# Performance work log

Measured on AMD Instinct MI355X. Metric: run time of the kernel, lower is better.

## Reference

```python
import jax, jax.numpy as jnp
import numpy as np

WS = 128          # crop window size
EPS = 1e-06


def setup_inputs() -> dict:
    key = jax.random.key(0)
    ks = jax.random.split(key, 8)
    E, S, K, H, W, HID = 32, 2, 256, 384, 384, 128
    x = jax.random.normal(ks[0], (E, H, W), jnp.float32)
    sigma = jax.random.uniform(ks[1], (S, H, W), jnp.float32)
    c = jax.random.normal(ks[2], (K, E), jnp.float32)
    centroids = jax.random.randint(ks[3], (K, 2), 0, H).astype(jnp.int32)
    M = jax.random.uniform(ks[4], (K, K), jnp.float32)  # sigmoid affinities in [0,1]
    din = E + S
    W1 = jax.random.normal(ks[5], (din, HID), jnp.float32) / np.sqrt(din)
    W2 = jax.random.normal(ks[6], (HID, HID), jnp.float32) / np.sqrt(HID)
    W3 = jax.random.normal(ks[7], (HID, 1), jnp.float32) / np.sqrt(HID)
    return {"x": x, "sigma": sigma, "c": c, "centroids": centroids, "M": M,
            "W1": W1, "b1": jnp.zeros((HID,), jnp.float32),
            "W2": W2, "b2": jnp.zeros((HID,), jnp.float32),
            "W3": W3, "b3": jnp.zeros((1,), jnp.float32)}


def reference(x, sigma, c, M, W1, b1, W2, b2, W3, b3, centroids):
    E, h, w = x.shape
    K = c.shape[0]
    ws, half = WS, WS // 2

    # ---- centre_crop: per-seed clamped top-left + mesh-grid indices ----
    cy = jnp.clip(centroids[:, 0], half, h - half)           # [K]
    cx = jnp.clip(centroids[:, 1], half, w - half)
    ty, tx = cy - half, cx - half                             # top-left (y, x)
    ar = jnp.arange(ws, dtype=jnp.int32)
    gy = jnp.broadcast_to(ty[:, None, None] + ar[None, :, None], (K, ws, ws))
    gx = jnp.broadcast_to(tx[:, None, None] + ar[None, None, :], (K, ws, ws))

    # ---- feature_engineering: gather crops, subtract seed embedding ----
    feats = jnp.concatenate([x, sigma], axis=0)               # [E+S, h, w]
    crops = feats[:, gy, gx]                                  # [E+S, K, ws, ws]
    crops = jnp.moveaxis(crops, 0, 1)                         # [K, E+S, ws, ws]
    crops = crops.at[:, :E].add(-c[:, :, None, None])

    # ---- pixel_classifier: per-pixel MLP -> logit ----
    pix = jnp.moveaxis(crops, 1, -1)                          # [K, ws, ws, E+S]
    h1 = jax.nn.relu(pix @ W1 + b1)
    h2 = jax.nn.relu(h1 @ W2 + b2)
    dist = (h2 @ W3 + b3)[..., 0]                             # [K, ws, ws]

    # ---- _gate_by_center_logit: logit(sig(a)*sig(b)) = a+b-softplus(logaddexp(a,b)) ----
    cyi = (centroids[:, 0] - ty).astype(jnp.int32)
    cxi = (centroids[:, 1] - tx).astype(jnp.int32)
    center = dist[jnp.arange(K), cyi, cxi]                    # [K]
    b = center[:, None, None]
    dist = dist + b - jax.nn.softplus(jnp.logaddexp(dist, b))

    # ---- apply_seed_merging: scatter to [K, h*w], affinity-weighted merge, gather ----
    Ms = 0.5 * (M + M.T)
    Ms = Ms.at[jnp.diag_indices(K)].set(1.0)
    pix_idx = (gy * w + gx).reshape(K, ws * ws)               # unique within each crop
    rows = jnp.arange(K)[:, None]
    logits = jnp.zeros((K, h * w), dist.dtype).at[rows, pix_idx].set(dist.reshape(K, -1))
    has = jnp.zeros((K, h * w), dist.dtype).at[rows, pix_idx].set(1.0)
    merged = (Ms @ logits) / jnp.clip(Ms @ has, EPS, None)
    out = merged[rows, pix_idx].reshape(K, 1, ws, ws)
    return out
```

## Files before the change

### kernel.cpp

```cpp
#include <hip/hip_runtime.h>
#include <hip/hip_bf16.h>


#define HH    384
#define WW    384
#define NE    32
#define NK    256
#define HALF  64
#define HWSZ  (HH * WW)
#define EPSV  1e-6f
#define CAPX  192

typedef _Float16 half8 __attribute__((ext_vector_type(8)));
typedef _Float16 half2v __attribute__((ext_vector_type(2)));
typedef float floatx4 __attribute__((ext_vector_type(4)));

#define MFMA16(a, b, c) __builtin_amdgcn_mfma_f32_16x16x32_f16((a), (b), (c), 0, 0, 0)

__device__ __forceinline__ half2v pk_f16(float a, float b) {
    return __builtin_bit_cast(half2v, __builtin_amdgcn_cvt_pkrtz(a, b));
}

__device__ __forceinline__ int row_order(int ri) {
    return (ri & 1) ? (191 - (ri >> 1)) : (192 + (ri >> 1));
}

#define WS_DIST   0
#define WS_MSYM   4194304
#define WS_W2F    4259840
#define WS_D      4268032
#define WS_CENTER 4284416
#define WS_G      5026560

__global__ void prep_kernel(const float* __restrict__ M, const float* __restrict__ W1,
                            const float* __restrict__ W2, const float* __restrict__ c,
                            const float* __restrict__ b1,
                            float* __restrict__ Msym, _Float16* __restrict__ W2f,
                            _Float16* __restrict__ D) {
    int idx = blockIdx.x * 256 + threadIdx.x;
    {
        int i = idx >> 8, j = idx & 255;
        Msym[idx] = (i == j) ? 1.0f : 0.5f * (M[i * NK + j] + M[j * NK + i]);
    }
    if (idx < 2048) {
        int l = idx & 63;
        int col = ((idx >> 8) << 4) + (l & 15);
        int kb = ((idx >> 6) & 3) * 32 + 8 * (l >> 4);
        #pragma unroll
        for (int j = 0; j < 8; ++j)
            W2f[idx * 8 + j] = (_Float16)W2[(kb + j) * 128 + col];
    }
    if (idx < 32768) {
        int k = idx >> 7, h = idx & 127;
        float s = -b1[h];
        #pragma unroll 8
        for (int e = 0; e < NE; ++e) s = fmaf(c[k * NE + e], W1[e * 128 + h], s);
        D[idx] = (_Float16)s;
    }
}

__global__ __launch_bounds__(256)
void gfeat_kernel(const float* __restrict__ x, const float* __restrict__ sigma,
                  const float* __restrict__ W1, _Float16* __restrict__ G) {
    int px = blockIdx.x * 256 + threadIdx.x;
    float f[34];
    #pragma unroll
    for (int e = 0; e < NE; ++e) f[e] = x[e * HWSZ + px];
    f[32] = sigma[px];
    f[33] = sigma[HWSZ + px];
    _Float16* gp = G + (size_t)px * 128;
    #pragma unroll 1
    for (int h0 = 0; h0 < 128; h0 += 8) {
        half8 hv;
        #pragma unroll
        for (int j = 0; j < 8; ++j) {
            float z = 0.0f;
            const float* w1 = W1 + (h0 + j);
            #pragma unroll
            for (int e = 0; e < 34; ++e) z = fmaf(f[e], w1[e * 128], z);
            hv[j] = (_Float16)z;
        }
        *(half8*)(gp + h0) = hv;
    }
}

__global__ __launch_bounds__(128)
void center2_kernel(const _Float16* __restrict__ G, const _Float16* __restrict__ D,
                    const float* __restrict__ W2, const float* __restrict__ b2,
                    const float* __restrict__ W3, const float* __restrict__ b3,
                    const int* __restrict__ cent, float* __restrict__ center) {
    __shared__ float h1s[128];
    __shared__ float red[2];
    int k = blockIdx.x, j = threadIdx.x;
    int cy0 = cent[2 * k], cx0 = cent[2 * k + 1];
    const _Float16* g = G + ((size_t)cy0 * WW + cx0) * 128;
    h1s[j] = fmaxf((float)g[j] - (float)D[k * 128 + j], 0.0f);
    __syncthreads();
    float acc = 0.0f;
    #pragma unroll 8
    for (int i = 0; i < 128; ++i) acc = fmaf(h1s[i], W2[i * 128 + j], acc);
    float p = fmaxf(acc + b2[j], 0.0f) * W3[j];
    #pragma unroll
    for (int m = 1; m < 64; m <<= 1) p += __shfl_xor(p, m, 64);
    if ((j & 63) == 0) red[j >> 6] = p;
    __syncthreads();
    if (j == 0) center[k] = red[0] + red[1] + b3[0];
}

__global__ __launch_bounds__(256)
void pix_kernel(const _Float16* __restrict__ G, const _Float16* __restrict__ D,
                const _Float16* __restrict__ W2f, const int* __restrict__ cent,
                const float* __restrict__ b2, const float* __restrict__ W3,
                const float* __restrict__ b3, const float* __restrict__ center,
                float* __restrict__ dist) {
    __shared__ int   sjw[CAPX];
    __shared__ float sctr[CAPX];
    __shared__ int   scnt;

    const int tid = threadIdx.x;
    const int l   = tid & 63;
    const int wv  = tid >> 6;
    const int lg  = l >> 4;
    const int xi  = l & 15;

    const int r   = row_order(blockIdx.x / 6);
    const int xt  = blockIdx.x % 6;
    const int wx0 = xt * 64 + wv * 16;

    if (wv == 0) {
        int base = 0;
        const int2* c2 = (const int2*)cent;
        #pragma unroll
        for (int cch = 0; cch < 4; ++cch) {
            int j = cch * 64 + l;
            int2 cc = c2[j];
            int ty = min(max(cc.x, HALF), HH - HALF) - HALF;
            int tx = min(max(cc.y, HALF), WW - HALF) - HALF;
            bool f = (r >= ty) && (r < ty + 128) &&
                     (tx <= xt * 64 + 63) && (tx + 127 >= xt * 64);
            unsigned long long m = __ballot(f);
            int pos = base + __popcll(m & ((1ull << l) - 1ull));
            if (f && pos < CAPX) {
                sjw[pos]  = (j << 20) | (ty << 10) | tx;
                sctr[pos] = center[j];
            }
            base += __popcll(m);
        }
        if (l == 0) scnt = min(base, CAPX);
    }

    half8 B2w[8][4];
    const half8* W2f8 = (const half8*)W2f;
    #pragma unroll
    for (int n = 0; n < 8; ++n)
        #pragma unroll
        for (int s = 0; s < 4; ++s) B2w[n][s] = W2f8[(n * 4 + s) * 64 + l];

    float b2v[8][4];
    half2v w3pk[8][2];
    #pragma unroll
    for (int n = 0; n < 8; ++n) {
        #pragma unroll
        for (int q = 0; q < 4; ++q) b2v[n][q] = b2[16 * n + 4 * lg + q];
        #pragma unroll
        for (int q = 0; q < 2; ++q)
            w3pk[n][q] = half2v{(_Float16)W3[16 * n + 4 * lg + 2 * q],
                                (_Float16)W3[16 * n + 4 * lg + 2 * q + 1]};
    }
    const float b3s = b3[0];

    half8 gA[4];
    {
        const char* Gb = (const char*)G + ((size_t)r * WW + wx0 + xi) * 256 + lg * 16;
        #pragma unroll
        for (int s = 0; s < 4; ++s) gA[s] = *(const half8*)(Gb + s * 64);
    }
    const half8 hz = half8{};
    __syncthreads();
    const int ncand = scnt;

    #pragma unroll 1
    for (int i = 0; i < ncand; ++i) {
        int cp = sjw[i];
        int tx = cp & 1023, ty = (cp >> 10) & 1023, j = cp >> 20;
        if (tx > wx0 + 15 || tx + 127 < wx0) continue;

        const char* Dp = (const char*)D + j * 256 + lg * 16;
        half8 hin[4];
        #pragma unroll
        for (int s = 0; s < 4; ++s) {
            half8 dv = *(const half8*)(Dp + s * 64);
            hin[s] = __builtin_elementwise_max(gA[s] - dv, hz);
        }

        float p = 0.0f;
        #pragma unroll
        for (int n = 0; n < 8; ++n) {
            floatx4 acc = floatx4{b2v[n][0], b2v[n][1], b2v[n][2], b2v[n][3]};
            #pragma unroll
            for (int s = 0; s < 4; ++s)
                acc = MFMA16(B2w[n][s], hin[s], acc);
            half2v h0 = __builtin_elementwise_max(pk_f16(acc[0], acc[1]), half2v{});
            half2v h1 = __builtin_elementwise_max(pk_f16(acc[2], acc[3]), half2v{});
            p = __builtin_amdgcn_fdot2(h0, w3pk[n][0], p, false);
            p = __builtin_amdgcn_fdot2(h1, w3pk[n][1], p, false);
        }
        p += __shfl_xor(p, 16, 64);
        p += __shfl_xor(p, 32, 64);

        if (lg == 0) {
            int xcol = wx0 + xi;
            unsigned dx = (unsigned)(xcol - tx);
            if (dx < 128u) {
                float d = p + b3s;
                float bc = sctr[i];
                float mm = fmaxf(fmaxf(d, bc), 0.0f);
                float lgv = mm + __logf(__expf(0.0f - mm) + __expf(d - mm) +
                                        __expf(bc - mm));
                dist[((size_t)j << 14) + ((r - ty) << 7) + (int)dx] = d + bc - lgv;
            }
        }
    }
}

__global__ __launch_bounds__(256)
void merge_kernel(const float* __restrict__ dist, const int* __restrict__ cent,
                  const float* __restrict__ Msym, float* __restrict__ out) {
    __shared__ _Float16 dl[CAPX][64];
    __shared__ int   sjw[CAPX];
    __shared__ int2  mpk[4][CAPX];
    __shared__ int   scnt;

    const int tid = threadIdx.x;
    const int l   = tid & 63;
    const int wv  = tid >> 6;
    const int r   = row_order(blockIdx.x / 6);
    const int xt  = blockIdx.x % 6;
    const int px  = xt * 64 + l;

    if (wv == 0) {
        int base = 0;
        const int2* c2 = (const int2*)cent;
        #pragma unroll
        for (int cch = 0; cch < 4; ++cch) {
            int j = cch * 64 + l;
            int2 cc = c2[j];
            int ty = min(max(cc.x, HALF), HH - HALF) - HALF;
            int tx = min(max(cc.y, HALF), WW - HALF) - HALF;
            bool f = (r >= ty) && (r < ty + 128) &&
                     (tx <= xt * 64 + 63) && (tx + 127 >= xt * 64);
            unsigned long long m = __ballot(f);
            int pos = base + __popcll(m & ((1ull << l) - 1ull));
            if (f && pos < CAPX) sjw[pos] = (j << 20) | (ty << 10) | tx;
            base += __popcll(m);
        }
        if (l == 0) scnt = min(base, CAPX);
    }
    __syncthreads();
    const int nc = scnt;

    #pragma unroll 1
    for (int j = wv; j < nc; j += 4) {
        int cp = sjw[j];
        int tx = cp & 1023, ty = (cp >> 10) & 1023, jj = cp >> 20;
        unsigned dx = (unsigned)(px - tx);
        float v = 0.0f;
        if (dx < 128u) v = dist[((size_t)jj << 14) + ((r - ty) << 7) + (int)dx];
        dl[j][l] = (_Float16)v;
    }
    __syncthreads();

    #pragma unroll 1
    for (int t = wv; t < nc; t += 4) {
        int cpt = sjw[t];
        int kt = cpt >> 20;
        const float* mrow = Msym + kt * NK;
        #pragma unroll
        for (int cch = 0; cch < 3; ++cch) {
            int j2 = cch * 64 + l;
            if (j2 < nc) {
                int cj = sjw[j2];
                mpk[wv][j2] = int2{__builtin_bit_cast(int, mrow[cj >> 20]),
                                   cj & 1023};
            }
        }
        float num = 0.0f, den = 0.0f;
        #pragma unroll 4
        for (int j = 0; j < nc; ++j) {
            int2 mp = mpk[wv][j];
            float m = __builtin_bit_cast(float, mp.x);
            num = fmaf(m, (float)dl[j][l], num);
            unsigned dxj = (unsigned)(px - mp.y);
            den += (dxj < 128u) ? m : 0.0f;
        }
        unsigned dxk = (unsigned)(px - (cpt & 1023));
        if (dxk < 128u)
            out[((size_t)kt << 14) + ((r - ((cpt >> 10) & 1023)) << 7) + (int)dxk] =
                num / fmaxf(den, EPSV);
    }
}

extern "C" void kernel_launch(void* const* d_in, const int* in_sizes, int n_in,
                              void* d_out, int out_size, void* d_ws, size_t ws_size,
                              hipStream_t stream) {
    const float* x     = (const float*)d_in[0];
    const float* sigma = (const float*)d_in[1];
    const float* c     = (const float*)d_in[2];
    const int*   cent  = (const int*)d_in[3];
    const float* M     = (const float*)d_in[4];
    const float* W1    = (const float*)d_in[5];
    const float* b1    = (const float*)d_in[6];
    const float* W2    = (const float*)d_in[7];
    const float* b2    = (const float*)d_in[8];
    const float* W3    = (const float*)d_in[9];
    const float* b3    = (const float*)d_in[10];
    float* out = (float*)d_out;

    float* ws       = (float*)d_ws;
    float* dist     = ws + WS_DIST;
    float* Msym     = ws + WS_MSYM;
    _Float16* W2f   = (_Float16*)(ws + WS_W2F);
    _Float16* D     = (_Float16*)(ws + WS_D);
    float* center   = ws + WS_CENTER;
    _Float16* G     = (_Float16*)(ws + WS_G);

    prep_kernel<<<256, 256, 0, stream>>>(M, W1, W2, c, b1, Msym, W2f, D);
    gfeat_kernel<<<576, 256, 0, stream>>>(x, sigma, W1, G);
    center2_kernel<<<256, 128, 0, stream>>>(G, D, W2, b2, W3, b3, cent, center);
    pix_kernel<<<2304, 256, 0, stream>>>(G, D, W2f, cent, b2, W3, b3, center, dist);
    merge_kernel<<<2304, 256, 0, stream>>>(dist, cent, Msym, out);
}
```

Before: 331.8 us.

## Stage W2 in LDS, build per-wave candidate lists, add bias in fp16

The W2 fragments move from 128 VGPRs per lane into a 32KB LDS buffer filled cooperatively by the block, which frees registers so more waves can be resident. Each wave now builds its own candidate list filtered on its 16-column strip, which removes the per-iteration column skip and the shared count. The b2 bias is added after packing to fp16 rather than seeding the fp32 accumulator, and s_setprio brackets the MFMA section. The costs are extra LDS reads on every MFMA, higher LDS use per block, a slight precision loss from the fp16 bias add, and every wave now scanning all centroids.

Result: no change. 331.8 us (+0.0%).

```diff
diff --git a/kernel.cpp b/kernel.cpp
--- a/kernel.cpp
+++ b/kernel.cpp
@@ -113,9 +113,9 @@
                 const float* __restrict__ b2, const float* __restrict__ W3,
                 const float* __restrict__ b3, const float* __restrict__ center,
                 float* __restrict__ dist) {
-    __shared__ int   sjw[CAPX];
-    __shared__ float sctr[CAPX];
-    __shared__ int   scnt;
+    __shared__ __align__(16) _Float16 w2l[16384];
+    __shared__ int   sjw[4][CAPX];
+    __shared__ float sctr[4][CAPX];
 
     const int tid = threadIdx.x;
     const int l   = tid & 63;
@@ -127,7 +127,15 @@
     const int xt  = blockIdx.x % 6;
     const int wx0 = xt * 64 + wv * 16;
 
-    if (wv == 0) {
+    {
+        const int4* src = (const int4*)W2f;
+        int4* dst = (int4*)w2l;
+        #pragma unroll
+        for (int q = 0; q < 8; ++q) dst[tid + 256 * q] = src[tid + 256 * q];
+    }
+
+    int nc;
+    {
         int base = 0;
         const int2* c2 = (const int2*)cent;
         #pragma unroll
@@ -137,36 +145,27 @@
             int ty = min(max(cc.x, HALF), HH - HALF) - HALF;
             int tx = min(max(cc.y, HALF), WW - HALF) - HALF;
             bool f = (r >= ty) && (r < ty + 128) &&
-                     (tx <= xt * 64 + 63) && (tx + 127 >= xt * 64);
+                     (tx <= wx0 + 15) && (tx + 127 >= wx0);
             unsigned long long m = __ballot(f);
             int pos = base + __popcll(m & ((1ull << l) - 1ull));
             if (f && pos < CAPX) {
-                sjw[pos]  = (j << 20) | (ty << 10) | tx;
-                sctr[pos] = center[j];
+                sjw[wv][pos]  = (j << 20) | (ty << 10) | tx;
+                sctr[wv][pos] = center[j];
             }
             base += __popcll(m);
         }
-        if (l == 0) scnt = min(base, CAPX);
-    }
-
-    half8 B2w[8][4];
-    const half8* W2f8 = (const half8*)W2f;
+        nc = min(base, CAPX);
+    }
+
+    half2v b2pk[8][2], w3pk[8][2];
     #pragma unroll
     for (int n = 0; n < 8; ++n)
         #pragma unroll
-        for (int s = 0; s < 4; ++s) B2w[n][s] = W2f8[(n * 4 + s) * 64 + l];
-
-    float b2v[8][4];
-    half2v w3pk[8][2];
-    #pragma unroll
-    for (int n = 0; n < 8; ++n) {
-        #pragma unroll
-        for (int q = 0; q < 4; ++q) b2v[n][q] = b2[16 * n + 4 * lg + q];
-        #pragma unroll
-        for (int q = 0; q < 2; ++q)
-            w3pk[n][q] = half2v{(_Float16)W3[16 * n + 4 * lg + 2 * q],
-                                (_Float16)W3[16 * n + 4 * lg + 2 * q + 1]};
-    }
+        for (int q = 0; q < 2; ++q) {
+            int o = 16 * n + 4 * lg + 2 * q;
+            b2pk[n][q] = half2v{(_Float16)b2[o], (_Float16)b2[o + 1]};
+            w3pk[n][q] = half2v{(_Float16)W3[o], (_Float16)W3[o + 1]};
+        }
     const float b3s = b3[0];
 
     half8 gA[4];
@@ -176,16 +175,18 @@
         for (int s = 0; s < 4; ++s) gA[s] = *(const half8*)(Gb + s * 64);
     }
     const half8 hz = half8{};
-    __syncthreads();
-    const int ncand = scnt;
+    const char* Dc = (const char*)D;
+
+    __syncthreads();
+    const half8* B2l = (const half8*)w2l;
 
     #pragma unroll 1
-    for (int i = 0; i < ncand; ++i) {
-        int cp = sjw[i];
+    for (int i = 0; i < nc; ++i) {
+        int cp = sjw[wv][i];
+        float bc = sctr[wv][i];
         int tx = cp & 1023, ty = (cp >> 10) & 1023, j = cp >> 20;
-        if (tx > wx0 + 15 || tx + 127 < wx0) continue;
-
-        const char* Dp = (const char*)D + j * 256 + lg * 16;
+
+        const char* Dp = Dc + j * 256 + lg * 16;
         half8 hin[4];
         #pragma unroll
         for (int s = 0; s < 4; ++s) {
@@ -194,17 +195,19 @@
         }
 
         float p = 0.0f;
+        __builtin_amdgcn_s_setprio(1);
         #pragma unroll
         for (int n = 0; n < 8; ++n) {
-            floatx4 acc = floatx4{b2v[n][0], b2v[n][1], b2v[n][2], b2v[n][3]};
+            floatx4 acc = floatx4{0.0f, 0.0f, 0.0f, 0.0f};
             #pragma unroll
             for (int s = 0; s < 4; ++s)
-                acc = MFMA16(B2w[n][s], hin[s], acc);
-            half2v h0 = __builtin_elementwise_max(pk_f16(acc[0], acc[1]), half2v{});
-            half2v h1 = __builtin_elementwise_max(pk_f16(acc[2], acc[3]), half2v{});
+                acc = MFMA16(B2l[(n * 4 + s) * 64 + l], hin[s], acc);
+            half2v h0 = __builtin_elementwise_max(pk_f16(acc[0], acc[1]) + b2pk[n][0], half2v{});
+            half2v h1 = __builtin_elementwise_max(pk_f16(acc[2], acc[3]) + b2pk[n][1], half2v{});
             p = __builtin_amdgcn_fdot2(h0, w3pk[n][0], p, false);
             p = __builtin_amdgcn_fdot2(h1, w3pk[n][1], p, false);
         }
+        __builtin_amdgcn_s_setprio(0);
         p += __shfl_xor(p, 16, 64);
         p += __shfl_xor(p, 32, 64);
 
@@ -213,7 +216,6 @@
             unsigned dx = (unsigned)(xcol - tx);
             if (dx < 128u) {
                 float d = p + b3s;
-                float bc = sctr[i];
                 float mm = fmaxf(fmaxf(d, bc), 0.0f);
                 float lgv = mm + __logf(__expf(0.0f - mm) + __expf(d - mm) +
                                         __expf(bc - mm));
```
